# Kernel optimization log

Measured on AMD Instinct MI355X. Metric: run time of the kernel, lower is better.

Reference implementation:

```python
import jax, jax.numpy as jnp
import numpy as np

EPS = 1e-5


def conv2d(x, w, stride=1, pad=1, b=None):
    out = jax.lax.conv_general_dilated(
        x, w, (stride, stride), [(pad, pad), (pad, pad)],
        dimension_numbers=('NCHW', 'OIHW', 'NCHW'))
    if b is not None:
        out = out + b[None, :, None, None]
    return out


def batchnorm(x, g, b):
    # training-mode BN (torch default): batch statistics over (N, H, W)
    m = x.mean((0, 2, 3), keepdims=True)
    v = x.var((0, 2, 3), keepdims=True)
    return (x - m) * jax.lax.rsqrt(v + EPS) * g[None, :, None, None] + b[None, :, None, None]


def deform(x, w_off):
    # ConvOffset2D: learn (B, 2C, H, W) offsets, bilinearly resample x per channel.
    B, C, H, W = x.shape
    off = conv2d(x, w_off, 1, 1)                 # (B, 2C, H, W)
    off = off.reshape(B * C, H * W, 2)           # matches torch row-major view to (B*C, H, W, 2)
    ii, jj = jnp.meshgrid(jnp.arange(H), jnp.arange(W), indexing='ij')
    grid = jnp.stack([ii, jj], -1).reshape(H * W, 2).astype(x.dtype)
    coords = off + grid[None]                    # absolute sample coords
    ci = jnp.clip(coords[..., 0], 0.0, H - 1)
    cj = jnp.clip(coords[..., 1], 0.0, W - 1)
    i0 = jnp.floor(ci)
    i1 = jnp.ceil(ci)
    j0 = jnp.floor(cj)
    j1 = jnp.ceil(cj)
    xf = x.reshape(B * C, H * W)

    def gather(iy, jx):
        idx = (iy * W + jx).astype(jnp.int32)
        return jnp.take_along_axis(xf, idx, axis=1)

    v00 = gather(i0, j0)
    v10 = gather(i1, j0)
    v01 = gather(i0, j1)
    v11 = gather(i1, j1)
    di = ci - i0
    dj = cj - j0
    top = v00 + di * (v10 - v00)   # interpolate along rows
    bot = v01 + di * (v11 - v01)
    out = top + dj * (bot - top)   # then along cols
    return out.reshape(B, C, H, W)


def setup_inputs() -> dict:
    key = jax.random.key(0)
    ks = jax.random.split(key, 24)
    f32 = jnp.float32
    d = {
        'x': jax.random.normal(ks[0], (64, 1, 112, 112), dtype=f32),
        'w11': jax.random.normal(ks[1], (32, 1, 3, 3), dtype=f32) * 0.1,
        'b11': jnp.zeros((32,), f32),
        'g11': jnp.ones((32,), f32),
        'be11': jnp.zeros((32,), f32),
        'woff12': jax.random.normal(ks[2], (64, 32, 3, 3), dtype=f32) * 0.01,
        'w12': jax.random.normal(ks[3], (64, 32, 3, 3), dtype=f32) * 0.1,
        'b12': jnp.zeros((64,), f32),
        'g12': jnp.ones((64,), f32),
        'be12': jnp.zeros((64,), f32),
        'woff21': jax.random.normal(ks[4], (128, 64, 3, 3), dtype=f32) * 0.01,
        'w21': jax.random.normal(ks[5], (128, 64, 3, 3), dtype=f32) * 0.1,
        'b21': jnp.zeros((128,), f32),
        'g21': jnp.ones((128,), f32),
        'be21': jnp.zeros((128,), f32),
        'woff22': jax.random.normal(ks[6], (256, 128, 3, 3), dtype=f32) * 0.01,
        'w22': jax.random.normal(ks[7], (128, 128, 3, 3), dtype=f32) * 0.1,
        'b22': jnp.zeros((128,), f32),
        'g22': jnp.ones((128,), f32),
        'be22': jnp.zeros((128,), f32),
        'wfc': jax.random.normal(ks[8], (10, 128), dtype=f32) * 0.1,
        'bfc': jnp.zeros((10,), f32),
    }
    return d


def reference(x, w11, b11, g11, be11, woff12, w12, b12, g12, be12,
              woff21, w21, b21, g21, be21, woff22, w22, b22, g22, be22,
              wfc, bfc):
    x = batchnorm(jax.nn.relu(conv2d(x, w11, 1, 1, b11)), g11, be11)
    x = deform(x, woff12)
    x = batchnorm(jax.nn.relu(conv2d(x, w12, 2, 1, b12)), g12, be12)
    x = deform(x, woff21)
    x = batchnorm(jax.nn.relu(conv2d(x, w21, 1, 1, b21)), g21, be21)
    x = deform(x, woff22)
    x = batchnorm(jax.nn.relu(conv2d(x, w22, 2, 1, b22)), g22, be22)
    x = x.mean((2, 3))                       # global avg pool -> (B, 128)
    logits = x @ wfc.T + bfc
    return jax.nn.softmax(logits, axis=1)
```

## Files before the change

kernel.cpp:

```cpp
#include <hip/hip_runtime.h>
#include <math.h>

#define BN_EPS 1e-5f

typedef unsigned short ushort_t;
typedef unsigned int uint_t;
typedef _Float16 half_t;
typedef __attribute__((ext_vector_type(8))) short short8;
typedef __attribute__((ext_vector_type(8))) _Float16 half8;
typedef __attribute__((ext_vector_type(4))) unsigned uint4v;
typedef __attribute__((ext_vector_type(2))) unsigned uint2v;
typedef __attribute__((ext_vector_type(16))) float floatx16;

__device__ __forceinline__ void split_bf16(float v, ushort_t& h, ushort_t& l) {
    unsigned u = __float_as_uint(v);
    float fhi = __uint_as_float(u & 0xFFFF0000u);
    h = (ushort_t)(u >> 16);
    l = (ushort_t)(__float_as_uint(v - fhi) >> 16);
}

__device__ __forceinline__ uint_t split_word(float v) {
    ushort_t h, l;
    split_bf16(v, h, l);
    return ((uint_t)h << 16) | (uint_t)l;
}

__device__ __forceinline__ float h2f_lo(uint_t u) {
    union { ushort_t s; half_t h; } cv; cv.s = (ushort_t)(u & 0xFFFFu);
    return (float)cv.h;
}
__device__ __forceinline__ float h2f_hi(uint_t u) {
    union { ushort_t s; half_t h; } cv; cv.s = (ushort_t)(u >> 16);
    return (float)cv.h;
}

__global__ __launch_bounds__(256) void prep_w_kernel(
    const float* __restrict__ w, ushort_t* __restrict__ hi,
    ushort_t* __restrict__ lo, int O, int I)
{
    int idx = blockIdx.x * 256 + threadIdx.x;
    int n = 9 * O * I;
    if (idx >= n) return;
    int i = idx % I;
    int rest = idx / I;
    int o = rest % O;
    int t = rest / O;
    float v = w[((size_t)o * I + i) * 9 + t];
    size_t d = ((((size_t)t * (O / 32) + (o >> 5)) * (I / 8) + (i >> 3)) * 32
                + (o & 31)) * 8 + (i & 7);
    split_bf16(v, hi[d], lo[d]);
}

__global__ __launch_bounds__(256) void prep_wf16_kernel(
    const float* __restrict__ w, half_t* __restrict__ o, int O, int I)
{
    int idx = blockIdx.x * 256 + threadIdx.x;
    int n = 9 * O * I;
    if (idx >= n) return;
    int i = idx % I;
    int rest = idx / I;
    int oo = rest % O;
    int t = rest / O;
    float v = w[((size_t)oo * I + i) * 9 + t];
    size_t d = ((((size_t)t * (O / 32) + (oo >> 5)) * (I / 8) + (i >> 3)) * 32
                + (oo & 31)) * 8 + (i & 7);
    o[d] = (half_t)v;
}

__global__ __launch_bounds__(256) void pack_af16_kernel(
    const float* __restrict__ x, const float* __restrict__ aff,
    half_t* __restrict__ xt, half_t* __restrict__ xl,
    int C, int HW, int total)
{
    int idx = blockIdx.x * 256 + threadIdx.x;
    if (idx >= total) return;
    int p = idx % HW;
    int rest = idx / HW;
    int cg = rest % (C / 8);
    int b  = rest / (C / 8);
    const float* xp = x + ((size_t)b * C + cg * 8) * HW + p;
    half8 hv;
    #pragma unroll
    for (int j = 0; j < 8; j++) {
        int c = cg * 8 + j;
        float v = fmaf(xp[(size_t)j * HW], aff[2 * c], aff[2 * c + 1]);
        hv[j] = (half_t)v;
        xl[((size_t)b * C + c) * HW + p] = hv[j];
    }
    size_t base = (size_t)b * C * HW + ((size_t)(p >> 5) * (C / 8) + cg) * 256
                + (size_t)(p & 31) * 8;
    *(half8*)(xt + base) = hv;
}

__global__ void bn_finalize_kernel(
    const float* __restrict__ stats, const float* __restrict__ g,
    const float* __restrict__ be, float inv_cnt, float* __restrict__ aff, int C)
{
    int c = threadIdx.x;
    if (c < C) {
        float m  = stats[c] * inv_cnt;
        float vv = stats[C + c] * inv_cnt - m * m;
        float sc = g[c] / sqrtf(vv + BN_EPS);
        aff[2 * c]     = sc;
        aff[2 * c + 1] = be[c] - m * sc;
    }
}

template<int W, int H, int CIN, int CO, int NT, int NZ>
__global__ __launch_bounds__(512, 4) void mfma_deform_g(
    const half_t* __restrict__ xt, const half_t* __restrict__ xl,
    const half_t* __restrict__ wf, uint_t* __restrict__ outp)
{
    constexpr int HWi = W * H;
    constexpr int KB  = CIN / 8;
    constexpr int TILES = HWi / 32;
    constexpr int XTB = (TILES + 7) / 8;
    constexpr int PER = XTB * NZ;
    constexpr int PITCH = 68;
    constexpr int QGH = HWi / 64;
    constexpr int NC2 = CIN / 16;
    constexpr int NCH = 9 * NT;
    constexpr int NPASS = (NCH + 7) / 8;
    constexpr int BUFB = NCH * 1024;
    constexpr size_t EPIB = 8 * (16 * PITCH * 8) + 8 * 1024;
    constexpr size_t LDSB = (2 * (size_t)BUFB > EPIB) ? 2 * (size_t)BUFB : EPIB;
    const half8 zero8 = {0, 0, 0, 0, 0, 0, 0, 0};

    __shared__ __align__(16) char ldsb[LDSB];

    const int tid  = threadIdx.x;
    const int wv   = tid >> 6;
    const int lane = tid & 63;
    const int l31  = lane & 31;
    const int kg   = lane >> 5;

    const int bid   = blockIdx.x;
    const int xcd   = bid & 7;
    const int s     = bid >> 3;
    const int kslot = s / PER;
    const int inner = s % PER;
    const int xti   = inner % XTB;
    const int zz    = inner / XTB;
    const int n0t   = zz * NT;
    const int b     = xcd * 8 + kslot;
    const int t0r   = xti * 8 + wv;
    const bool act  = t0r < TILES;
    const int t0    = act ? t0r : TILES - 1;

    const int mp = t0 * 32 + l31;
    const int py = mp / W, px = mp % W;
    const size_t xtb = (size_t)b * CIN * HWi;

    unsigned aoff[9];
    unsigned amask = 0;
    #pragma unroll
    for (int ki = 0; ki < 3; ki++) {
        #pragma unroll
        for (int kj = 0; kj < 3; kj++) {
            int t  = ki * 3 + kj;
            int iy = py + ki - 1, ix = px + kj - 1;
            bool v = (iy >= 0 && iy < H && ix >= 0 && ix < W);
            int ps = v ? iy * W + ix : 0;
            aoff[t] = (unsigned)((ps >> 5) * KB * 256 + (ps & 31) * 8);
            amask |= (v ? 1u : 0u) << t;
        }
    }

    floatx16 acc[NT];
    #pragma unroll
    for (int i = 0; i < NT; i++)
        #pragma unroll
        for (int j = 0; j < 16; j++) acc[i][j] = 0.f;

    auto stage = [&](int c2s, int buf) {
        #pragma unroll
        for (int it = 0; it < NPASS; it++) {
            int slot  = it * 8 + wv;
            int chunk = slot < NCH ? slot : slot - NCH;
            int t  = chunk / NT;
            int nt = chunk % NT;
            const half_t* src = wf
                + (((size_t)t * (CO / 32) + (n0t + nt)) * KB + (size_t)c2s * 2) * 256
                + lane * 8;
            __builtin_amdgcn_global_load_lds(
                (const __attribute__((address_space(1))) unsigned*)src,
                (__attribute__((address_space(3))) unsigned*)(ldsb + buf * BUFB + chunk * 1024),
                16, 0, 0);
        }
    };

    stage(0, 0);
    asm volatile("s_waitcnt vmcnt(0)" ::: "memory");
    __syncthreads();

    for (int c2 = 0; c2 < NC2; c2++) {
        const int cur = c2 & 1;
        if (c2 + 1 < NC2) stage(c2 + 1, cur ^ 1);
        const unsigned kb = c2 * 2 + kg;
        #pragma unroll
        for (int t = 0; t < 9; t++) {
            const size_t au = xtb + aoff[t] + (size_t)kb * 256;
            half8 a = *(const half8*)(xt + au);
            if (!((amask >> t) & 1u)) a = zero8;
            #pragma unroll
            for (int nt = 0; nt < NT; nt++) {
                const half8 bv = *(const half8*)(ldsb + cur * BUFB
                                 + (t * NT + nt) * 1024 + kg * 512 + l31 * 16);
                acc[nt] = __builtin_amdgcn_mfma_f32_32x32x16_f16(a, bv, acc[nt], 0, 0, 0);
            }
        }
        if (c2 + 1 < NC2) {
            asm volatile("s_waitcnt vmcnt(0)" ::: "memory");
            __syncthreads();
        }
    }

    __syncthreads();

    if (!act) return;

    float2* offw = (float2*)(ldsb + (size_t)wv * (16 * PITCH * 8));
    uint_t* stgw = (uint_t*)(ldsb + 8 * (16 * PITCH * 8) + (size_t)wv * 1024);
    const int qb  = (t0 & 1) * 16;
    const int qg0 = t0 >> 1;

    #pragma unroll
    for (int half = 0; half < NT / 2; half++) {
        #pragma unroll
        for (int ntl = 0; ntl < 2; ntl++) {
            const int gl = ntl * 32 + l31;
            #pragma unroll
            for (int t = 0; t < 8; t++) {
                int r2w = (t & 1) + 2 * kg + 4 * (t >> 1);
                offw[r2w * PITCH + gl] =
                    float2{acc[half * 2 + ntl][2 * t], acc[half * 2 + ntl][2 * t + 1]};
            }
        }
        asm volatile("s_waitcnt lgkmcnt(0)" ::: "memory");

        const int bc0 = n0t * 16 + half * 32;
        #pragma unroll
        for (int sc = 0; sc < 4; sc++) {
            const int r2 = lane & 15;
            #pragma unroll
            for (int sub = 0; sub < 4; sub++) {
                const int gl  = sc * 16 + sub * 4 + (lane >> 4);
                float2 od = offw[r2 * PITCH + gl];
                const int hlf = (lane >> 4) & 1;
                const int c   = bc0 + sc * 8 + sub * 2 + kg;
                const int q   = hlf * (HWi / 2) + t0 * 16 + r2;
                const int qi = q / W, qj = q % W;
                float ci_ = fminf(fmaxf(od.x + (float)qi, 0.f), (float)(H - 1));
                float cj_ = fminf(fmaxf(od.y + (float)qj, 0.f), (float)(W - 1));
                float i0f = floorf(ci_), j0f = floorf(cj_);
                int i0 = (int)i0f, i1 = (int)ceilf(ci_);
                int j0 = (int)j0f;
                const half_t* gp = xl + xtb + (size_t)c * HWi;
                uint_t u0 = *(const uint_t*)(gp + i0 * W + j0);
                uint_t u1 = *(const uint_t*)(gp + i1 * W + j0);
                float v00 = h2f_lo(u0), v01 = h2f_hi(u0);
                float v10 = h2f_lo(u1), v11 = h2f_hi(u1);
                float di = ci_ - i0f, dj = cj_ - j0f;
                float top = v00 + di * (v10 - v00);
                float bot = v01 + di * (v11 - v01);
                float res = top + dj * (bot - top);
                stgw[hlf * 128 + r2 * 8 + (sub * 2 + kg)] = split_word(res);
            }
            asm volatile("s_waitcnt lgkmcnt(0)" ::: "memory");
            const int cg = (bc0 >> 3) + sc;
            #pragma unroll
            for (int hlf = 0; hlf < 2; hlf++) {
                uint2v dd = *(const uint2v*)&stgw[hlf * 128 + 2 * lane];
                size_t dst = xtb + ((size_t)(hlf * QGH + qg0) * KB + cg) * 256
                           + (size_t)qb * 8 + 2 * lane;
                *(uint2v*)(outp + dst) = dd;
            }
        }
    }
}

template<int S, int W, int H, int CIN, int CO, int NT, int XT, int NZ>
__global__ __launch_bounds__(128, 2) void mfma_conv_g(
    const uint_t* __restrict__ xt,
    const ushort_t* __restrict__ wh, const ushort_t* __restrict__ wl,
    const float* __restrict__ bias, float* __restrict__ out)
{
    constexpr int Wo  = W / S, Ho = H / S;
    constexpr int HWo = Wo * Ho;
    constexpr int HWi = W * H;
    constexpr int KB  = CIN / 8;
    constexpr int PER = XT * NZ;

    const int tid  = threadIdx.x;
    const int wv   = tid >> 6;
    const int lane = tid & 63;
    const int l31  = lane & 31;
    const int kg   = lane >> 5;

    const int bid   = blockIdx.x;
    const int xcd   = bid & 7;
    const int s     = bid >> 3;
    const int k     = s / PER;
    const int inner = s % PER;
    const int b     = xcd * 8 + k;
    const int xti   = inner % XT;
    const int zz    = inner / XT;
    const int n0t   = zz * NT;
    const int t0    = xti * 2 + wv;

    const int mp  = t0 * 32 + l31;
    const int mpc = mp < HWo ? mp : HWo - 1;
    const int py  = mpc / Wo, px = mpc % Wo;
    const size_t xtb = (size_t)b * CIN * HWi;

    unsigned aoff[9];
    unsigned amask = 0;
    #pragma unroll
    for (int ki = 0; ki < 3; ki++) {
        #pragma unroll
        for (int kj = 0; kj < 3; kj++) {
            int t  = ki * 3 + kj;
            int iy = py * S + ki - 1, ix = px * S + kj - 1;
            bool v = (iy >= 0 && iy < H && ix >= 0 && ix < W);
            int ps = v ? iy * W + ix : 0;
            aoff[t] = (unsigned)((ps >> 5) * KB * 256 + (ps & 31) * 8);
            amask |= (v ? 1u : 0u) << t;
        }
    }

    floatx16 acc[NT];
    #pragma unroll
    for (int i = 0; i < NT; i++)
        #pragma unroll
        for (int j = 0; j < 16; j++) acc[i][j] = 0.f;

    for (int c2 = 0; c2 < CIN / 16; c2++) {
        const unsigned kb = c2 * 2 + kg;
        #pragma unroll
        for (int t = 0; t < 9; t++) {
            const size_t au = xtb + aoff[t] + (size_t)kb * 256;
            uint4v w0 = *(const uint4v*)(xt + au);
            uint4v w1 = *(const uint4v*)(xt + au + 4);
            if (!((amask >> t) & 1u)) {
                w0 = uint4v{0, 0, 0, 0};
                w1 = uint4v{0, 0, 0, 0};
            }
            union { short8 s; uint_t u[4]; } uh, ul;
            uh.u[0] = (w0.x >> 16) | (w0.y & 0xFFFF0000u);
            uh.u[1] = (w0.z >> 16) | (w0.w & 0xFFFF0000u);
            uh.u[2] = (w1.x >> 16) | (w1.y & 0xFFFF0000u);
            uh.u[3] = (w1.z >> 16) | (w1.w & 0xFFFF0000u);
            ul.u[0] = (w0.x & 0xFFFFu) | (w0.y << 16);
            ul.u[1] = (w0.z & 0xFFFFu) | (w0.w << 16);
            ul.u[2] = (w1.x & 0xFFFFu) | (w1.y << 16);
            ul.u[3] = (w1.z & 0xFFFFu) | (w1.w << 16);
            short8 ah = uh.s, al = ul.s;
            #pragma unroll
            for (int nt = 0; nt < NT; nt++) {
                const size_t bofs =
                    ((((size_t)t * (CO / 32) + (n0t + nt)) * KB + kb) * 32 + l31) * 8;
                short8 bh = *(const short8*)(wh + bofs);
                short8 bl = *(const short8*)(wl + bofs);
                floatx16 a = acc[nt];
                a = __builtin_amdgcn_mfma_f32_32x32x16_bf16(ah, bh, a, 0, 0, 0);
                a = __builtin_amdgcn_mfma_f32_32x32x16_bf16(ah, bl, a, 0, 0, 0);
                a = __builtin_amdgcn_mfma_f32_32x32x16_bf16(al, bh, a, 0, 0, 0);
                acc[nt] = a;
            }
        }
    }

    #pragma unroll
    for (int nt = 0; nt < NT; nt++) {
        int co = (n0t + nt) * 32 + l31;
        float bv = bias[co];
        #pragma unroll
        for (int reg = 0; reg < 16; reg++) {
            int row = (reg & 3) + 8 * (reg >> 2) + 4 * kg;
            int p   = t0 * 32 + row;
            if (p < HWo)
                out[((size_t)b * CO + co) * HWo + p] = fmaxf(acc[nt][reg] + bv, 0.f);
        }
    }
}

template<int STRIDE>
__global__ __launch_bounds__(256) void conv3x3_kernel(
    const float* __restrict__ in, const float* __restrict__ wgt,
    const float* __restrict__ bias, float* __restrict__ out,
    int B, int Cin, int H, int W, int Cout, int Ho, int Wo, int do_relu)
{
    constexpr int TILE = 28;
    constexpr int PR   = (TILE - 1) * STRIDE + 3;
    constexpr int PADW = (STRIDE == 1) ? 32 : 60;
    constexpr int COPB = 8;
    constexpr int RW   = STRIDE + 3;
    __shared__ float patch[PR * PADW];

    int cpg  = Cout / COPB;
    int bz   = blockIdx.z;
    int cog  = bz % cpg;
    int b    = bz / cpg;
    int co0  = cog * COPB;
    int tid  = threadIdx.x;
    int oy0  = blockIdx.y * TILE, ox0 = blockIdx.x * TILE;
    int iy0  = oy0 * STRIDE - 1,  ix0 = ox0 * STRIDE - 1;

    bool active = tid < 196;
    int ty = tid / 14, tx = tid % 14;
    int py = oy0 + 2 * ty, px = ox0 + 2 * tx;

    float acc[COPB][4];
    #pragma unroll
    for (int i = 0; i < COPB; i++) {
        float bv = bias ? bias[co0 + i] : 0.f;
        #pragma unroll
        for (int j = 0; j < 4; j++) acc[i][j] = bv;
    }

    const size_t HW = (size_t)H * W;
    for (int ci = 0; ci < Cin; ci++) {
        const float* ip = in + ((size_t)b * Cin + ci) * HW;
        for (int t = tid; t < PR * PADW; t += 256) {
            int sy = t / PADW, sx = t % PADW;
            float v = 0.f;
            int gy = iy0 + sy, gx = ix0 + sx;
            if (sx < PR && gy >= 0 && gy < H && gx >= 0 && gx < W)
                v = ip[(size_t)gy * W + gx];
            patch[t] = v;
        }
        __syncthreads();
        if (active) {
            float r[RW][RW];
            #pragma unroll
            for (int rr = 0; rr < RW; rr++) {
                int rowbase = (2 * ty * STRIDE + rr) * PADW + 2 * tx * STRIDE;
                if (STRIDE == 1) {
                    float2 a = *(const float2*)&patch[rowbase];
                    float2 c = *(const float2*)&patch[rowbase + 2];
                    r[rr][0] = a.x; r[rr][1] = a.y; r[rr][2] = c.x; r[rr][3] = c.y;
                } else {
                    float4 a = *(const float4*)&patch[rowbase];
                    r[rr][0] = a.x; r[rr][1] = a.y; r[rr][2] = a.z; r[rr][3] = a.w;
                    r[rr][4] = patch[rowbase + 4];
                }
            }
            const float* wb = wgt + ((size_t)co0 * Cin + ci) * 9;
            #pragma unroll
            for (int i = 0; i < COPB; i++) {
                const float* wp = wb + (size_t)i * Cin * 9;
                #pragma unroll
                for (int ki = 0; ki < 3; ki++)
                    #pragma unroll
                    for (int kj = 0; kj < 3; kj++) {
                        float w = wp[ki * 3 + kj];
                        acc[i][0] = fmaf(r[ki][kj],                   w, acc[i][0]);
                        acc[i][1] = fmaf(r[ki][kj + STRIDE],          w, acc[i][1]);
                        acc[i][2] = fmaf(r[ki + STRIDE][kj],          w, acc[i][2]);
                        acc[i][3] = fmaf(r[ki + STRIDE][kj + STRIDE], w, acc[i][3]);
                    }
            }
        }
        __syncthreads();
    }
    if (active) {
        #pragma unroll
        for (int rr = 0; rr < 2; rr++) {
            #pragma unroll
            for (int cc = 0; cc < 2; cc++) {
                int oy = py + rr, ox = px + cc;
                if (oy < Ho && ox < Wo) {
                    #pragma unroll
                    for (int i = 0; i < COPB; i++) {
                        float v = acc[i][rr * 2 + cc];
                        if (do_relu) v = fmaxf(v, 0.f);
                        out[(((size_t)b * Cout + co0 + i) * Ho + oy) * Wo + ox] = v;
                    }
                }
            }
        }
    }
}

__global__ __launch_bounds__(256) void bn_stats_kernel(
    const float* __restrict__ x, float* __restrict__ stats,
    int B, int C, int HW)
{
    int c = blockIdx.x;
    long long cnt = (long long)B * HW;
    long long step = (long long)gridDim.y * blockDim.x;
    float s = 0.f, s2 = 0.f;
    for (long long t = (long long)blockIdx.y * blockDim.x + threadIdx.x; t < cnt; t += step) {
        int b  = (int)(t / HW);
        int sp = (int)(t % HW);
        float v = x[((size_t)b * C + c) * (size_t)HW + sp];
        s += v; s2 += v * v;
    }
    for (int off = 32; off; off >>= 1) {
        s  += __shfl_down(s, off);
        s2 += __shfl_down(s2, off);
    }
    __shared__ float ls[4], ls2[4];
    int wave = threadIdx.x >> 6, lane = threadIdx.x & 63;
    if (lane == 0) { ls[wave] = s; ls2[wave] = s2; }
    __syncthreads();
    if (threadIdx.x == 0) {
        float ts = 0.f, ts2 = 0.f;
        for (int i = 0; i < 4; i++) { ts += ls[i]; ts2 += ls2[i]; }
        atomicAdd(&stats[c], ts);
        atomicAdd(&stats[C + c], ts2);
    }
}

__global__ void zero_kernel(float* __restrict__ p, int n)
{
    int i = blockIdx.x * blockDim.x + threadIdx.x;
    if (i < n) p[i] = 0.f;
}

__global__ __launch_bounds__(256) void pool_kernel(
    const float* __restrict__ x, const float* __restrict__ stats,
    const float* __restrict__ g, const float* __restrict__ be,
    float inv_cnt, float* __restrict__ out, int C, int HW)
{
    int bc = blockIdx.x;
    int c  = bc % C;
    const float* xp = x + (size_t)bc * HW;
    float s = 0.f;
    for (int i = threadIdx.x; i < HW; i += blockDim.x) s += xp[i];
    for (int off = 32; off; off >>= 1) s += __shfl_down(s, off);
    __shared__ float ls[4];
    int wave = threadIdx.x >> 6, lane = threadIdx.x & 63;
    if (lane == 0) ls[wave] = s;
    __syncthreads();
    if (threadIdx.x == 0) {
        float t = 0.f;
        for (int i = 0; i < 4; i++) t += ls[i];
        float mean = t / (float)HW;
        float m  = stats[c] * inv_cnt;
        float vv = stats[C + c] * inv_cnt - m * m;
        float sc = g[c] / sqrtf(vv + BN_EPS);
        float sh = be[c] - m * sc;
        out[bc] = mean * sc + sh;
    }
}

__global__ __launch_bounds__(128) void fc_softmax_kernel(
    const float* __restrict__ pool, const float* __restrict__ wfc,
    const float* __restrict__ bfc, float* __restrict__ out)
{
    int b = blockIdx.x;
    __shared__ float row[128];
    __shared__ float logits[10];
    int tid = threadIdx.x;
    row[tid] = pool[b * 128 + tid];
    __syncthreads();
    if (tid < 10) {
        float s = bfc[tid];
        for (int k = 0; k < 128; k++) s = fmaf(row[k], wfc[tid * 128 + k], s);
        logits[tid] = s;
    }
    __syncthreads();
    if (tid < 10) {
        float mx = logits[0];
        for (int i = 1; i < 10; i++) mx = fmaxf(mx, logits[i]);
        float sum = 0.f;
        for (int i = 0; i < 10; i++) sum += expf(logits[i] - mx);
        out[b * 10 + tid] = expf(logits[tid] - mx) / sum;
    }
}

extern "C" void kernel_launch(void* const* d_in, const int* in_sizes, int n_in,
                              void* d_out, int out_size, void* d_ws, size_t ws_size,
                              hipStream_t stream)
{
    const float* x      = (const float*)d_in[0];
    const float* w11    = (const float*)d_in[1];
    const float* b11    = (const float*)d_in[2];
    const float* g11    = (const float*)d_in[3];
    const float* be11   = (const float*)d_in[4];
    const float* woff12 = (const float*)d_in[5];
    const float* w12    = (const float*)d_in[6];
    const float* b12    = (const float*)d_in[7];
    const float* g12    = (const float*)d_in[8];
    const float* be12   = (const float*)d_in[9];
    const float* woff21 = (const float*)d_in[10];
    const float* w21    = (const float*)d_in[11];
    const float* b21    = (const float*)d_in[12];
    const float* g21    = (const float*)d_in[13];
    const float* be21   = (const float*)d_in[14];
    const float* woff22 = (const float*)d_in[15];
    const float* w22    = (const float*)d_in[16];
    const float* b22    = (const float*)d_in[17];
    const float* g22    = (const float*)d_in[18];
    const float* be22   = (const float*)d_in[19];
    const float* wfc    = (const float*)d_in[20];
    const float* bfc    = (const float*)d_in[21];
    float* out = (float*)d_out;

    float* ws    = (float*)d_ws;
    const size_t SZ_B = 25690112;

    float*  R0f = ws;
    uint_t* R0u = (uint_t*)R0f;
    half_t* R0h = (half_t*)R0f;
    half_t* R0l = R0h + SZ_B;
    float* stats = R0f + SZ_B;
    float* aff   = stats + 512;
    float* poolb = aff + 512;
    uint_t* R1u = (uint_t*)(poolb + 8192);
    float*  R1f = (float*)R1u;
    half_t* R1h = (half_t*)R1u;
    half_t* R1l = R1h + SZ_B;
    ushort_t* warena = (ushort_t*)(R1u + SZ_B);
    const size_t W12 = 9 * 64 * 32;
    const size_t W21 = 9 * 128 * 64;
    const size_t W22c = 9 * 128 * 128;
    const size_t W12o = 9 * 64 * 32;
    const size_t W21o = 9 * 128 * 64;
    ushort_t* wc12h = warena;          ushort_t* wc12l = wc12h + W12;
    ushort_t* wc21h = wc12l + W12;     ushort_t* wc21l = wc21h + W21;
    ushort_t* wc22h = wc21l + W21;     ushort_t* wc22l = wc22h + W22c;
    half_t* wpf12 = (half_t*)(wc22l + W22c);
    half_t* wpf21 = wpf12 + W12o;
    half_t* wpf22 = wpf21 + W21o;

    const int B = 64;

    prep_w_kernel<<<(9*64*32   + 255)/256, 256, 0, stream>>>(w12, wc12h, wc12l, 64, 32);
    prep_w_kernel<<<(9*128*64  + 255)/256, 256, 0, stream>>>(w21, wc21h, wc21l, 128, 64);
    prep_w_kernel<<<(9*128*128 + 255)/256, 256, 0, stream>>>(w22, wc22h, wc22l, 128, 128);
    prep_wf16_kernel<<<(9*64*32   + 255)/256, 256, 0, stream>>>(woff12, wpf12, 64, 32);
    prep_wf16_kernel<<<(9*128*64  + 255)/256, 256, 0, stream>>>(woff21, wpf21, 128, 64);
    prep_wf16_kernel<<<(9*256*128 + 255)/256, 256, 0, stream>>>(woff22, wpf22, 256, 128);

    conv3x3_kernel<1><<<dim3(4, 4, B * (32 / 8)), 256, 0, stream>>>(
        x, w11, b11, R0f, B, 1, 112, 112, 32, 112, 112, 1);
    zero_kernel<<<2, 256, 0, stream>>>(stats, 512);
    bn_stats_kernel<<<dim3(32, 64), 256, 0, stream>>>(R0f, stats, B, 32, 12544);
    bn_finalize_kernel<<<1, 256, 0, stream>>>(stats, g11, be11, 1.f/(64.f*12544.f), aff, 32);

    pack_af16_kernel<<<(B*4*12544 + 255)/256, 256, 0, stream>>>(
        R0f, aff, R1h, R1l, 32, 12544, B*4*12544);
    mfma_deform_g<112, 112, 32, 64, 2, 1>
        <<<dim3(64 * 49), 512, 0, stream>>>(R1h, R1l, wpf12, R0u);

    mfma_conv_g<2, 112, 112, 32, 64, 2, 49, 1>
        <<<dim3(49 * B), 128, 0, stream>>>(R0u, wc12h, wc12l, b12, R1f);
    zero_kernel<<<2, 256, 0, stream>>>(stats, 512);
    bn_stats_kernel<<<dim3(64, 64), 256, 0, stream>>>(R1f, stats, B, 64, 3136);
    bn_finalize_kernel<<<1, 256, 0, stream>>>(stats, g12, be12, 1.f/(64.f*3136.f), aff, 64);

    pack_af16_kernel<<<(B*8*3136 + 255)/256, 256, 0, stream>>>(
        R1f, aff, R0h, R0l, 64, 3136, B*8*3136);
    mfma_deform_g<56, 56, 64, 128, 4, 1>
        <<<dim3(64 * 13), 512, 0, stream>>>(R0h, R0l, wpf21, R1u);

    mfma_conv_g<1, 56, 56, 64, 128, 4, 49, 1>
        <<<dim3(49 * B), 128, 0, stream>>>(R1u, wc21h, wc21l, b21, R0f);
    zero_kernel<<<2, 256, 0, stream>>>(stats, 512);
    bn_stats_kernel<<<dim3(128, 64), 256, 0, stream>>>(R0f, stats, B, 128, 3136);
    bn_finalize_kernel<<<1, 256, 0, stream>>>(stats, g21, be21, 1.f/(64.f*3136.f), aff, 128);

    pack_af16_kernel<<<(B*16*3136 + 255)/256, 256, 0, stream>>>(
        R0f, aff, R1h, R1l, 128, 3136, B*16*3136);
    mfma_deform_g<56, 56, 128, 256, 4, 2>
        <<<dim3(64 * 26), 512, 0, stream>>>(R1h, R1l, wpf22, R0u);

    mfma_conv_g<2, 56, 56, 128, 128, 4, 13, 1>
        <<<dim3(13 * B), 128, 0, stream>>>(R0u, wc22h, wc22l, b22, R1f);
    zero_kernel<<<2, 256, 0, stream>>>(stats, 512);
    bn_stats_kernel<<<dim3(128, 64), 256, 0, stream>>>(R1f, stats, B, 128, 784);

    pool_kernel<<<B * 128, 256, 0, stream>>>(
        R1f, stats, g22, be22, 1.f/(64.f*784.f), poolb, 128, 784);
    fc_softmax_kernel<<<B, 128, 0, stream>>>(poolb, wfc, bfc, out);
}
```

Before: 1.173 ms.

## Stage conv weights in LDS with double-buffered async loads, 8-wave blocks

The split-bf16 MFMA conv now runs 512-thread blocks where 8 waves share one output-channel group. Per input-channel chunk, the weight tiles are copied into LDS with global_load_lds and double-buffered, so the next chunk loads while the current one computes. Before, every wave read weights from global memory on its own, so this cuts redundant weight traffic. The cost is block-wide barriers, a larger LDS footprint, smaller NT on two layers, and idle waves on partial tiles.

```diff
diff --git a/kernel.cpp b/kernel.cpp
--- a/kernel.cpp
+++ b/kernel.cpp
@@ -279,8 +279,8 @@
     }
 }
 
-template<int S, int W, int H, int CIN, int CO, int NT, int XT, int NZ>
-__global__ __launch_bounds__(128, 2) void mfma_conv_g(
+template<int S, int W, int H, int CIN, int CO, int NT, int NZ>
+__global__ __launch_bounds__(512, 4) void mfma_conv_g(
     const uint_t* __restrict__ xt,
     const ushort_t* __restrict__ wh, const ushort_t* __restrict__ wl,
     const float* __restrict__ bias, float* __restrict__ out)
@@ -289,7 +289,15 @@
     constexpr int HWo = Wo * Ho;
     constexpr int HWi = W * H;
     constexpr int KB  = CIN / 8;
-    constexpr int PER = XT * NZ;
+    constexpr int TILES = (HWo + 31) / 32;
+    constexpr int XTB = (TILES + 7) / 8;
+    constexpr int PER = XTB * NZ;
+    constexpr int NC2 = CIN / 16;
+    constexpr int NCH = 9 * NT * 2;
+    constexpr int NPASS = (NCH + 7) / 8;
+    constexpr int BUFB = NCH * 1024;
+
+    __shared__ __align__(16) char ldsb[2 * BUFB];
 
     const int tid  = threadIdx.x;
     const int wv   = tid >> 6;
@@ -300,13 +308,15 @@
     const int bid   = blockIdx.x;
     const int xcd   = bid & 7;
     const int s     = bid >> 3;
-    const int k     = s / PER;
+    const int kslot = s / PER;
     const int inner = s % PER;
-    const int b     = xcd * 8 + k;
-    const int xti   = inner % XT;
-    const int zz    = inner / XT;
+    const int xti   = inner % XTB;
+    const int zz    = inner / XTB;
     const int n0t   = zz * NT;
-    const int t0    = xti * 2 + wv;
+    const int b     = xcd * 8 + kslot;
+    const int t0r   = xti * 8 + wv;
+    const bool act  = t0r < TILES;
+    const int t0    = act ? t0r : TILES - 1;
 
     const int mp  = t0 * 32 + l31;
     const int mpc = mp < HWo ? mp : HWo - 1;
@@ -334,7 +344,32 @@
         #pragma unroll
         for (int j = 0; j < 16; j++) acc[i][j] = 0.f;
 
-    for (int c2 = 0; c2 < CIN / 16; c2++) {
+    auto stage = [&](int c2s, int buf) {
+        #pragma unroll
+        for (int it = 0; it < NPASS; it++) {
+            int slot  = it * 8 + wv;
+            int chunk = slot < NCH ? slot : slot - NCH;
+            int plane = chunk & 1;
+            int tn = chunk >> 1;
+            int t  = tn / NT;
+            int nt = tn % NT;
+            const ushort_t* srcp = (plane ? wl : wh)
+                + (((size_t)t * (CO / 32) + (n0t + nt)) * KB + (size_t)c2s * 2) * 256
+                + lane * 8;
+            __builtin_amdgcn_global_load_lds(
+                (const __attribute__((address_space(1))) unsigned*)srcp,
+                (__attribute__((address_space(3))) unsigned*)(ldsb + buf * BUFB + chunk * 1024),
+                16, 0, 0);
+        }
+    };
+
+    stage(0, 0);
+    asm volatile("s_waitcnt vmcnt(0)" ::: "memory");
+    __syncthreads();
+
+    for (int c2 = 0; c2 < NC2; c2++) {
+        const int cur = c2 & 1;
+        if (c2 + 1 < NC2) stage(c2 + 1, cur ^ 1);
         const unsigned kb = c2 * 2 + kg;
         #pragma unroll
         for (int t = 0; t < 9; t++) {
@@ -357,10 +392,10 @@
             short8 ah = uh.s, al = ul.s;
             #pragma unroll
             for (int nt = 0; nt < NT; nt++) {
-                const size_t bofs =
-                    ((((size_t)t * (CO / 32) + (n0t + nt)) * KB + kb) * 32 + l31) * 8;
-                short8 bh = *(const short8*)(wh + bofs);
-                short8 bl = *(const short8*)(wl + bofs);
+                const char* bb = ldsb + cur * BUFB
+                               + ((t * NT + nt) * 2) * 1024 + kg * 512 + l31 * 16;
+                short8 bh = *(const short8*)bb;
+                short8 bl = *(const short8*)(bb + 1024);
                 floatx16 a = acc[nt];
                 a = __builtin_amdgcn_mfma_f32_32x32x16_bf16(ah, bh, a, 0, 0, 0);
                 a = __builtin_amdgcn_mfma_f32_32x32x16_bf16(ah, bl, a, 0, 0, 0);
@@ -368,7 +403,13 @@
                 acc[nt] = a;
             }
         }
-    }
+        if (c2 + 1 < NC2) {
+            asm volatile("s_waitcnt vmcnt(0)" ::: "memory");
+            __syncthreads();
+        }
+    }
+
+    if (!act) return;
 
     #pragma unroll
     for (int nt = 0; nt < NT; nt++) {
@@ -645,8 +686,8 @@
     mfma_deform_g<112, 112, 32, 64, 2, 1>
         <<<dim3(64 * 49), 512, 0, stream>>>(R1h, R1l, wpf12, R0u);
 
-    mfma_conv_g<2, 112, 112, 32, 64, 2, 49, 1>
-        <<<dim3(49 * B), 128, 0, stream>>>(R0u, wc12h, wc12l, b12, R1f);
+    mfma_conv_g<2, 112, 112, 32, 64, 2, 1>
+        <<<dim3(64 * 13), 512, 0, stream>>>(R0u, wc12h, wc12l, b12, R1f);
     zero_kernel<<<2, 256, 0, stream>>>(stats, 512);
     bn_stats_kernel<<<dim3(64, 64), 256, 0, stream>>>(R1f, stats, B, 64, 3136);
     bn_finalize_kernel<<<1, 256, 0, stream>>>(stats, g12, be12, 1.f/(64.f*3136.f), aff, 64);
@@ -656,8 +697,8 @@
     mfma_deform_g<56, 56, 64, 128, 4, 1>
         <<<dim3(64 * 13), 512, 0, stream>>>(R0h, R0l, wpf21, R1u);
 
-    mfma_conv_g<1, 56, 56, 64, 128, 4, 49, 1>
-        <<<dim3(49 * B), 128, 0, stream>>>(R1u, wc21h, wc21l, b21, R0f);
+    mfma_conv_g<1, 56, 56, 64, 128, 2, 2>
+        <<<dim3(64 * 26), 512, 0, stream>>>(R1u, wc21h, wc21l, b21, R0f);
     zero_kernel<<<2, 256, 0, stream>>>(stats, 512);
     bn_stats_kernel<<<dim3(128, 64), 256, 0, stream>>>(R0f, stats, B, 128, 3136);
     bn_finalize_kernel<<<1, 256, 0, stream>>>(stats, g21, be21, 1.f/(64.f*3136.f), aff, 128);
@@ -667,8 +708,8 @@
     mfma_deform_g<56, 56, 128, 256, 4, 2>
         <<<dim3(64 * 26), 512, 0, stream>>>(R1h, R1l, wpf22, R0u);
 
-    mfma_conv_g<2, 56, 56, 128, 128, 4, 13, 1>
-        <<<dim3(13 * B), 128, 0, stream>>>(R0u, wc22h, wc22l, b22, R1f);
+    mfma_conv_g<2, 56, 56, 128, 128, 2, 2>
+        <<<dim3(64 * 8), 512, 0, stream>>>(R0u, wc22h, wc22l, b22, R1f);
     zero_kernel<<<2, 256, 0, stream>>>(stats, 512);
     bn_stats_kernel<<<dim3(128, 64), 256, 0, stream>>>(R1f, stats, B, 128, 784);
 
```

Result: faster. 1.041 ms (median of 2 runs) (-11.3%).
